# Kernel tuning notes

Hardware: AMD Instinct MI355X
Metric: run time of the kernel (lower is better)

The kernel has to match this reference:

```python
import jax, jax.numpy as jnp
import numpy as np

SENT_LEN, SENT_BATCH, WORD_LEN = 256, 64, 16
EMB, HID = 128, 256
CEMB, CHID = 64, 128
VOCAB, CVOCAB, TAGS = 50000, 128, 50


def setup_inputs() -> dict:
    key = jax.random.key(0)
    ks = jax.random.split(key, 14)
    s = 0.1  # param init scale, avoids gate saturation
    n = lambda k, shape: (jax.random.normal(k, shape, dtype=jnp.float32) * s)
    return {
        "sentences": jax.random.randint(ks[0], (SENT_LEN, SENT_BATCH), 0, VOCAB),
        "words": jax.random.randint(ks[1], (SENT_BATCH, WORD_LEN, SENT_LEN), 0, CVOCAB),
        "char_embedding_dim": CEMB,
        "char_hidden_dim": CHID,
        "word_emb": n(ks[2], (VOCAB, EMB)),
        "char_emb": n(ks[3], (CVOCAB, CEMB)),
        "Wih_c": n(ks[4], (4 * CHID, CEMB)),
        "Whh_c": n(ks[5], (4 * CHID, CHID)),
        "bih_c": n(ks[6], (4 * CHID,)),
        "bhh_c": n(ks[7], (4 * CHID,)),
        "Wih_w": n(ks[8], (4 * HID, EMB + CHID)),
        "Whh_w": n(ks[9], (4 * HID, HID)),
        "bih_w": n(ks[10], (4 * HID,)),
        "bhh_w": n(ks[11], (4 * HID,)),
        "W_tag": n(ks[12], (TAGS, HID)),
        "b_tag": n(ks[13], (TAGS,)),
    }


def _lstm_cell(h, c, x, Wih, Whh, b):
    # torch gate order: input, forget, cell(g), output
    gates = x @ Wih.T + h @ Whh.T + b
    i, f, g, o = jnp.split(gates, 4, axis=-1)
    c_new = jax.nn.sigmoid(f) * c + jax.nn.sigmoid(i) * jnp.tanh(g)
    h_new = jax.nn.sigmoid(o) * jnp.tanh(c_new)
    return h_new, c_new


def reference(sentences, words, char_embedding_dim, char_hidden_dim,
              word_emb, char_emb, Wih_c, Whh_c, bih_c, bhh_c,
              Wih_w, Whh_w, bih_w, bhh_w, W_tag, b_tag):
    sent_len, sent_batch = sentences.shape
    dt = word_emb.dtype

    embeds = word_emb[sentences]            # [T, B, EMB]
    ce = char_emb[words]                    # [B, WL, T, CEMB]

    # char LSTM: per sentence, seq=WL, batch=T; hidden carried ACROSS sentences
    b_c = bih_c + bhh_c

    def char_sentence(carry, sent_ce):      # sent_ce: [WL, T, CEMB]
        def step(hc, x):
            h, c = _lstm_cell(hc[0], hc[1], x, Wih_c, Whh_c, b_c)
            return (h, c), None
        carry, _ = jax.lax.scan(step, carry, sent_ce)
        return carry, carry[0]               # final h: [T, CHID]

    init_c = (jnp.zeros((sent_len, CHID), dt), jnp.zeros((sent_len, CHID), dt))
    _, char_finals = jax.lax.scan(char_sentence, init_c, ce)  # [B, T, CHID]
    char_finals = jnp.transpose(char_finals, (1, 0, 2))        # [T, B, CHID]

    x = jnp.concatenate([embeds, char_finals], axis=-1)        # [T, B, EMB+CHID]

    # word LSTM over time=T, batch=B
    b_w = bih_w + bhh_w

    def word_step(hc, xt):
        h, c = _lstm_cell(hc[0], hc[1], xt, Wih_w, Whh_w, b_w)
        return (h, c), h

    init_w = (jnp.zeros((sent_batch, HID), dt), jnp.zeros((sent_batch, HID), dt))
    _, lstm_out = jax.lax.scan(word_step, init_w, x)           # [T, B, HID]

    tag_space = lstm_out @ W_tag.T + b_tag                     # [T, B, TAGS]
    return jax.nn.log_softmax(tag_space, axis=-1)
```

## Files before the change

### kernel.cpp

```cpp
#include <hip/hip_runtime.h>
#include <hip/hip_bf16.h>
#include <cstdint>

#define SENT_LEN   256
#define SENT_BATCH 64
#define WORD_LEN   16
#define EMB        128
#define HID        256
#define CEMB       64
#define CHID       128
#define TAGS       50
#define K_IN       (EMB + CHID)
#define LOG2E      1.44269504f
#define N2LOG2E    -2.88539008f

typedef __attribute__((ext_vector_type(8))) short short8;
typedef __attribute__((ext_vector_type(4))) float f32x4;
typedef __attribute__((ext_vector_type(4))) int   i32x4;
typedef __attribute__((ext_vector_type(2))) long  lng2;

__device__ __forceinline__ float rcpf(float x) { return __builtin_amdgcn_rcpf(x); }
__device__ __forceinline__ float sig2(float xl) {
    return rcpf(1.f + __builtin_amdgcn_exp2f(-xl));
}
__device__ __forceinline__ float tanh2(float xl) {
    float e = __builtin_amdgcn_exp2f(-(xl + xl));
    return 2.f * rcpf(1.f + e) - 1.f;
}
__device__ __forceinline__ float lstm_act(float gi, float gf, float gg, float go, float& cst) {
    float c = sig2(gf) * cst + sig2(gi) * tanh2(gg);
    cst = c;
    float tc = 2.f * rcpf(1.f + __builtin_amdgcn_exp2f(N2LOG2E * c)) - 1.f;
    return sig2(go) * tc;
}
__device__ __forceinline__ float bf_lo(unsigned u) { return __uint_as_float(u << 16); }
__device__ __forceinline__ float bf_hi(unsigned u) { return __uint_as_float(u & 0xffff0000u); }
__device__ __forceinline__ unsigned short f2bfu(float f) {
    unsigned u = __float_as_uint(f);
    u += 0x7fff + ((u >> 16) & 1);
    return (unsigned short)(u >> 16);
}
__device__ __forceinline__ void block_sync_lds() {
    asm volatile("s_waitcnt lgkmcnt(0)\ns_barrier" ::: "memory");
}
__device__ __forceinline__ i32x4 mfma_i8_k64(lng2 a, lng2 b, i32x4 c) {
    i32x4 av = __builtin_bit_cast(i32x4, a);
    i32x4 bv = __builtin_bit_cast(i32x4, b);
    return __builtin_amdgcn_mfma_i32_16x16x64_i8(av, bv, c, 0, 0, 0);
}
template<int Q> __device__ __forceinline__ float qbcast(float x) {
    return __int_as_float(__builtin_amdgcn_mov_dpp(
        __float_as_int(x), Q * 0x55, 0xF, 0xF, false));
}

__global__ void prep_char(const float* __restrict__ Wih_c, const float* __restrict__ char_emb,
                          const float* __restrict__ bih_c, const float* __restrict__ bhh_c,
                          float* __restrict__ pre8) {
    int ch = blockIdx.x;
    int g  = threadIdx.x;
    float acc = bih_c[g] + bhh_c[g];
    const float4* w4 = reinterpret_cast<const float4*>(Wih_c + (size_t)g * CEMB);
    const float4* e4 = reinterpret_cast<const float4*>(char_emb + (size_t)ch * CEMB);
#pragma unroll
    for (int k = 0; k < CEMB / 4; k++) {
        float4 wv = w4[k], ev = e4[k];
        acc += wv.x * ev.x; acc += wv.y * ev.y;
        acc += wv.z * ev.z; acc += wv.w * ev.w;
    }
    int gt = g >> 7, j = g & 127;
    float s_e = (gt == 2) ? -2.f : -1.f;
    pre8[((ch * 128) + j) * 4 + gt] = acc * LOG2E * s_e;
}

__global__ void prep_wq(const float* __restrict__ Whh_w, const float* __restrict__ Wih_w,
                        signed char* __restrict__ wq, float* __restrict__ sw,
                        unsigned short* __restrict__ wihb) {
    int g = blockIdx.x;
    int lane = threadIdx.x;
    float4 v = reinterpret_cast<const float4*>(Whh_w + (size_t)g * HID)[lane];
    float m = fmaxf(fmaxf(fabsf(v.x), fabsf(v.y)), fmaxf(fabsf(v.z), fabsf(v.w)));
#pragma unroll
    for (int off = 32; off; off >>= 1) m = fmaxf(m, __shfl_xor(m, off, 64));
    m = fmaxf(m, 1e-20f);
    float inv = 127.f / m;
    int q0 = __float2int_rn(v.x * inv), q1 = __float2int_rn(v.y * inv);
    int q2 = __float2int_rn(v.z * inv), q3 = __float2int_rn(v.w * inv);
    int packed = (q0 & 255) | ((q1 & 255) << 8) | ((q2 & 255) << 16) | ((q3 & 255) << 24);
    reinterpret_cast<int*>(wq)[g * 64 + lane] = packed;
    if (lane == 0) sw[g] = m / 127.f;
    float4 wv = reinterpret_cast<const float4*>(Wih_w + (size_t)g * K_IN)[lane];
    uint2 p;
    p.x = (unsigned)f2bfu(wv.x) | ((unsigned)f2bfu(wv.y) << 16);
    p.y = (unsigned)f2bfu(wv.z) | ((unsigned)f2bfu(wv.w) << 16);
    int n2 = g >> 8, j = g & 255, jt = j >> 4, l15 = j & 15;
    int k0 = lane * 4;
    int kt = k0 >> 5, lqf = (k0 >> 3) & 3;
    size_t fidx = ((size_t)(jt * 4 + n2) * 8 + kt) * 64 + (lqf * 16 + l15);
    char* dst = (char*)wihb + fidx * 16 + (size_t)(k0 & 4) * 2;
    *reinterpret_cast<uint2*>(dst) = p;
}

__global__ __launch_bounds__(512, 1) void char_lstm(
        const int* __restrict__ words, const float* __restrict__ Whh_c,
        const float* __restrict__ pre8, const int* __restrict__ sentences,
        const float* __restrict__ word_emb, const unsigned short* __restrict__ wihb,
        const float* __restrict__ bih_w, const float* __restrict__ bhh_w,
        uint2* __restrict__ xw8) {
    int t    = blockIdx.x;
    int tid  = threadIdx.x;
    int lane = tid & 63, w = tid >> 6;
    int nt   = lane & 3;
    int j    = w * 16 + (lane >> 2);
    int g    = nt * 128 + j;

    __shared__ __align__(16) signed char hv[2][128];
    __shared__ __align__(16) unsigned short xls[64][264];

    const float4* wr = reinterpret_cast<const float4*>(Whh_c + (size_t)g * CHID);
    float mx = 1e-20f;
#pragma unroll
    for (int q = 0; q < 32; q++) {
        float4 f = wr[q];
        mx = fmaxf(mx, fmaxf(fmaxf(fabsf(f.x), fabsf(f.y)), fmaxf(fabsf(f.z), fabsf(f.w))));
    }
    float inv = 127.f / mx;
    int wqr[32];
#pragma unroll
    for (int q = 0; q < 32; q++) {
        float4 f = wr[q];
        wqr[q] = (__float2int_rn(f.x * inv) & 255)
               | ((__float2int_rn(f.y * inv) & 255) << 8)
               | ((__float2int_rn(f.z * inv) & 255) << 16)
               | ((__float2int_rn(f.w * inv) & 255) << 24);
    }
    float s_e   = (nt == 2) ? -2.f : -1.f;
    float swl_s = s_e * mx * (LOG2E / (127.f * 127.f));
    float m_a   = (nt == 2) ?  2.f :  1.f;
    float b_a   = (nt == 2) ? -1.f :  0.f;

    {
        int b  = tid >> 3;
        int c8 = tid & 7;
        int sid = sentences[t * 64 + b];
        const float4* ep = reinterpret_cast<const float4*>(
            word_emb + (size_t)sid * EMB + c8 * 16);
        float4 e0 = ep[0], e1 = ep[1], e2 = ep[2], e3 = ep[3];
        short8 v0, v1;
        v0[0] = (short)f2bfu(e0.x); v0[1] = (short)f2bfu(e0.y);
        v0[2] = (short)f2bfu(e0.z); v0[3] = (short)f2bfu(e0.w);
        v0[4] = (short)f2bfu(e1.x); v0[5] = (short)f2bfu(e1.y);
        v0[6] = (short)f2bfu(e1.z); v0[7] = (short)f2bfu(e1.w);
        v1[0] = (short)f2bfu(e2.x); v1[1] = (short)f2bfu(e2.y);
        v1[2] = (short)f2bfu(e2.z); v1[3] = (short)f2bfu(e2.w);
        v1[4] = (short)f2bfu(e3.x); v1[5] = (short)f2bfu(e3.y);
        v1[6] = (short)f2bfu(e3.z); v1[7] = (short)f2bfu(e3.w);
        *reinterpret_cast<short8*>(&xls[b][c8 * 16])     = v0;
        *reinterpret_cast<short8*>(&xls[b][c8 * 16 + 8]) = v1;
    }

    if (tid < 64) { reinterpret_cast<int*>(hv)[tid] = 0; }

    float cst = 0.f;
    int cid0 = words[t];
    int cid1 = words[SENT_LEN + t];
    float pl0 = pre8[(size_t)cid0 * 512 + tid];
    float pl1 = pre8[(size_t)cid1 * 512 + tid];
    int ci2 = words[2 * SENT_LEN + t];
    int ci3 = words[3 * SENT_LEN + t];
    __syncthreads();

    for (int u = 0; u < 512; u++) {
        float pf0 = pre8[(size_t)ci2 * 512 + tid];
        float pf1 = pre8[(size_t)ci3 * 512 + tid];
        ci2 = words[(((u << 1) + 4) & 1023) * SENT_LEN + t];
        ci3 = words[(((u << 1) + 5) & 1023) * SENT_LEN + t];

        {
            const i32x4* hp = reinterpret_cast<const i32x4*>(hv[0]);
            int a0 = 0, a1 = 0, a2 = 0, a3 = 0;
#pragma unroll
            for (int q = 0; q < 8; q++) {
                i32x4 hq = hp[q];
                a0 = __builtin_amdgcn_sdot4(hq.x, wqr[q * 4 + 0], a0, false);
                a1 = __builtin_amdgcn_sdot4(hq.y, wqr[q * 4 + 1], a1, false);
                a2 = __builtin_amdgcn_sdot4(hq.z, wqr[q * 4 + 2], a2, false);
                a3 = __builtin_amdgcn_sdot4(hq.w, wqr[q * 4 + 3], a3, false);
            }
            int s = (a0 + a1) + (a2 + a3);
            float e  = __builtin_amdgcn_exp2f(fmaf((float)s, swl_s, pl0));
            float av = m_a * rcpf(1.f + e) + b_a;
            float qi = qbcast<0>(av);
            float qf = qbcast<1>(av);
            float qg = qbcast<2>(av);
            float qo = qbcast<3>(av);
            float c  = fmaf(qf, cst, qi * qg);
            cst = c;
            float tc = 2.f * rcpf(1.f + __builtin_amdgcn_exp2f(N2LOG2E * c)) - 1.f;
            float h  = qo * tc;
            if (nt == 0)
                hv[1][j] = (signed char)__float2int_rn(h * 127.f);
            block_sync_lds();
        }
        {
            const i32x4* hp = reinterpret_cast<const i32x4*>(hv[1]);
            int a0 = 0, a1 = 0, a2 = 0, a3 = 0;
#pragma unroll
            for (int q = 0; q < 8; q++) {
                i32x4 hq = hp[q];
                a0 = __builtin_amdgcn_sdot4(hq.x, wqr[q * 4 + 0], a0, false);
                a1 = __builtin_amdgcn_sdot4(hq.y, wqr[q * 4 + 1], a1, false);
                a2 = __builtin_amdgcn_sdot4(hq.z, wqr[q * 4 + 2], a2, false);
                a3 = __builtin_amdgcn_sdot4(hq.w, wqr[q * 4 + 3], a3, false);
            }
            int s = (a0 + a1) + (a2 + a3);
            float e  = __builtin_amdgcn_exp2f(fmaf((float)s, swl_s, pl1));
            float av = m_a * rcpf(1.f + e) + b_a;
            float qi = qbcast<0>(av);
            float qf = qbcast<1>(av);
            float qg = qbcast<2>(av);
            float qo = qbcast<3>(av);
            float c  = fmaf(qf, cst, qi * qg);
            cst = c;
            float tc = 2.f * rcpf(1.f + __builtin_amdgcn_exp2f(N2LOG2E * c)) - 1.f;
            float h  = qo * tc;
            if (nt == 0) {
                hv[0][j] = (signed char)__float2int_rn(h * 127.f);
                if ((u & 7) == 7)
                    xls[u >> 3][128 + j] = f2bfu(h);
            }
            block_sync_lds();
        }
        pl0 = pf0; pl1 = pf1;
    }

    {
        int l15 = lane & 15, lq = lane >> 4;
        int mt  = w & 3;
        short8 af[8];
#pragma unroll
        for (int kt = 0; kt < 8; kt++)
            af[kt] = *reinterpret_cast<const short8*>(&xls[mt * 16 + l15][kt * 32 + lq * 8]);
        const short8* bF = reinterpret_cast<const short8*>(wihb);
#pragma unroll 1
        for (int jt = (w >> 2); jt < 16; jt += 2) {
            int j0 = jt * 16;
            const short8* bJ = bF + (size_t)jt * 4 * 8 * 64 + lane;
            f32x4 acc[4] = {{0.f,0.f,0.f,0.f},{0.f,0.f,0.f,0.f},
                            {0.f,0.f,0.f,0.f},{0.f,0.f,0.f,0.f}};
#pragma unroll
            for (int kt = 0; kt < 8; kt++) {
#pragma unroll
                for (int n2 = 0; n2 < 4; n2++) {
                    short8 bf = bJ[(n2 * 8 + kt) * 64];
                    acc[n2] = __builtin_amdgcn_mfma_f32_16x16x32_bf16(
                        af[kt], bf, acc[n2], 0, 0, 0);
                }
            }
            float bb[4];
#pragma unroll
            for (int n2 = 0; n2 < 4; n2++)
                bb[n2] = bih_w[n2 * 256 + j0 + l15] + bhh_w[n2 * 256 + j0 + l15];
#pragma unroll
            for (int r = 0; r < 4; r++) {
                int br = mt * 16 + lq * 4 + r;
                uint2 o;
                o.x = (unsigned)f2bfu((acc[0][r] + bb[0]) * LOG2E)
                    | ((unsigned)f2bfu((acc[1][r] + bb[1]) * LOG2E) << 16);
                o.y = (unsigned)f2bfu((acc[2][r] + bb[2]) * LOG2E)
                    | ((unsigned)f2bfu((acc[3][r] + bb[3]) * LOG2E) << 16);
                xw8[((size_t)br * SENT_LEN + t) * 256 + j0 + l15] = o;
            }
        }
    }
}

__global__ __launch_bounds__(1024, 1) void word_lstm(
        const uint2* __restrict__ xw8, const signed char* __restrict__ wq,
        const float* __restrict__ sw, float* __restrict__ h_out) {
    int b    = blockIdx.x;
    int tid  = threadIdx.x;
    int lane = tid & 63, w = tid >> 6;
    int l15  = lane & 15, lq = lane >> 4;
    int j    = w * 16 + l15;

    __shared__ __align__(16) signed char hv[2][256];

    lng2 bfr[4][4];
    float swl[4];
#pragma unroll
    for (int nt = 0; nt < 4; nt++) {
        int g = nt * 256 + j;
        swl[nt] = sw[g] * (LOG2E / 127.f);
#pragma unroll
        for (int kt = 0; kt < 4; kt++)
            bfr[nt][kt] = reinterpret_cast<const lng2*>(wq + (size_t)g * HID + kt * 64 + lq * 16)[0];
    }
    if (tid < 128) { reinterpret_cast<int*>(hv)[tid] = 0; }

    const uint2* xwb = xw8 + (size_t)b * SENT_LEN * 256;
    float cst = 0.f;
    uint2 xq0 = xwb[0 * 256 + j];
    uint2 xq1 = xwb[1 * 256 + j];
    uint2 xq2 = xwb[2 * 256 + j];
    uint2 xq3 = xwb[3 * 256 + j];
    __syncthreads();

    for (int u = 0; u < 128; u++) {
        uint2 xn0 = xwb[((((u << 1) + 4) & 255)) * 256 + j];
        uint2 xn1 = xwb[((((u << 1) + 5) & 255)) * 256 + j];

        {
            const lng2* hp = reinterpret_cast<const lng2*>(hv[0]);
            i32x4 acc[4] = {};
#pragma unroll
            for (int kt = 0; kt < 4; kt++) {
                lng2 a = hp[kt * 4 + lq];
#pragma unroll
                for (int nt = 0; nt < 4; nt++)
                    acc[nt] = mfma_i8_k64(a, bfr[nt][kt], acc[nt]);
            }
            float gi = (float)acc[0][0] * swl[0] + bf_lo(xq0.x);
            float gf = (float)acc[1][0] * swl[1] + bf_hi(xq0.x);
            float gg = (float)acc[2][0] * swl[2] + bf_lo(xq0.y);
            float go = (float)acc[3][0] * swl[3] + bf_hi(xq0.y);
            float h = lstm_act(gi, gf, gg, go, cst);
            if (lq == 0) {
                h_out[((size_t)(u << 1) * SENT_BATCH + b) * HID + j] = h;
                hv[1][j] = (signed char)__float2int_rn(h * 127.f);
            }
            block_sync_lds();
        }
        {
            const lng2* hp = reinterpret_cast<const lng2*>(hv[1]);
            i32x4 acc[4] = {};
#pragma unroll
            for (int kt = 0; kt < 4; kt++) {
                lng2 a = hp[kt * 4 + lq];
#pragma unroll
                for (int nt = 0; nt < 4; nt++)
                    acc[nt] = mfma_i8_k64(a, bfr[nt][kt], acc[nt]);
            }
            float gi = (float)acc[0][0] * swl[0] + bf_lo(xq1.x);
            float gf = (float)acc[1][0] * swl[1] + bf_hi(xq1.x);
            float gg = (float)acc[2][0] * swl[2] + bf_lo(xq1.y);
            float go = (float)acc[3][0] * swl[3] + bf_hi(xq1.y);
            float h = lstm_act(gi, gf, gg, go, cst);
            if (lq == 0) {
                h_out[((size_t)((u << 1) + 1) * SENT_BATCH + b) * HID + j] = h;
                hv[0][j] = (signed char)__float2int_rn(h * 127.f);
            }
            block_sync_lds();
        }
        xq0 = xq2; xq1 = xq3; xq2 = xn0; xq3 = xn1;
    }
}

__global__ __launch_bounds__(256) void tag_logsoftmax(
        const float* __restrict__ h_out, const float* __restrict__ W_tag,
        const float* __restrict__ b_tag, float* __restrict__ out) {
    __shared__ float wt_s[TAGS * 257];
    __shared__ float hr_s[8 * HID];
    int tid = threadIdx.x;
    int row0 = blockIdx.x * 8;
#pragma unroll 2
    for (int i = 0; i < TAGS; i++) wt_s[i * 257 + tid] = W_tag[i * HID + tid];
#pragma unroll
    for (int w = 0; w < 8; w++) hr_s[w * HID + tid] = h_out[(size_t)(row0 + w) * HID + tid];
    __syncthreads();

    int w4 = tid >> 6, l = tid & 63;
#pragma unroll
    for (int rep = 0; rep < 2; rep++) {
        int w = rep * 4 + w4;
        float acc = 0.f;
        if (l < TAGS) {
            acc = b_tag[l];
            const float* hr = hr_s + w * HID;
            const float* wr = wt_s + l * 257;
#pragma unroll 4
            for (int k = 0; k < HID; k++) acc += hr[k] * wr[k];
        }
        float m = (l < TAGS) ? acc : -1e30f;
#pragma unroll
        for (int off = 32; off; off >>= 1) m = fmaxf(m, __shfl_xor(m, off, 64));
        float e = (l < TAGS) ? __builtin_amdgcn_exp2f((acc - m) * LOG2E) : 0.f;
        float ssum = e;
#pragma unroll
        for (int off = 32; off; off >>= 1) ssum += __shfl_xor(ssum, off, 64);
        float lse = m + __logf(ssum);
        if (l < TAGS) out[(size_t)(row0 + w) * TAGS + l] = acc - lse;
    }
}

extern "C" void kernel_launch(void* const* d_in, const int* in_sizes, int n_in,
                              void* d_out, int out_size, void* d_ws, size_t ws_size,
                              hipStream_t stream) {
    (void)in_sizes; (void)n_in; (void)out_size; (void)ws_size;
    const int*   sentences = (const int*)d_in[0];
    const int*   words     = (const int*)d_in[1];
    const float* word_emb  = (const float*)d_in[4];
    const float* char_emb  = (const float*)d_in[5];
    const float* Wih_c     = (const float*)d_in[6];
    const float* Whh_c     = (const float*)d_in[7];
    const float* bih_c     = (const float*)d_in[8];
    const float* bhh_c     = (const float*)d_in[9];
    const float* Wih_w     = (const float*)d_in[10];
    const float* Whh_w     = (const float*)d_in[11];
    const float* bih_w     = (const float*)d_in[12];
    const float* bhh_w     = (const float*)d_in[13];
    const float* W_tag     = (const float*)d_in[14];
    const float* b_tag     = (const float*)d_in[15];
    float* out = (float*)d_out;

    char* ws = (char*)d_ws;
    size_t off = 0;
    float* pre8 = (float*)(ws + off);                 off += 128 * 512 * sizeof(float);
    signed char* wq = (signed char*)(ws + off);       off += 1024 * 256;
    float* sw = (float*)(ws + off);                   off += 1024 * sizeof(float);
    unsigned short* wihb = (unsigned short*)(ws + off); off += (size_t)1024 * K_IN * 2;
    off = (off + 255) & ~(size_t)255;
    uint2* xw8 = (uint2*)(ws + off);                  off += (size_t)SENT_LEN * SENT_BATCH * 256 * sizeof(uint2);
    float* h_out = (float*)(ws + off);                off += (size_t)SENT_LEN * SENT_BATCH * HID * sizeof(float);

    hipLaunchKernelGGL(prep_char, dim3(128), dim3(512), 0, stream,
                       Wih_c, char_emb, bih_c, bhh_c, pre8);
    hipLaunchKernelGGL(prep_wq, dim3(1024), dim3(64), 0, stream, Whh_w, Wih_w, wq, sw, wihb);
    hipLaunchKernelGGL(char_lstm, dim3(256), dim3(512), 0, stream,
                       words, Whh_c, pre8, sentences, word_emb, wihb, bih_w, bhh_w, xw8);
    hipLaunchKernelGGL(word_lstm, dim3(SENT_BATCH), dim3(1024), 0, stream,
                       xw8, wq, sw, h_out);
    hipLaunchKernelGGL(tag_logsoftmax, dim3((SENT_LEN * SENT_BATCH) / 8), dim3(256), 0, stream,
                       h_out, W_tag, b_tag, out);
}
```

Before: 808.8 us.

## Halve word LSTM block to 512 threads with two hidden units per thread; merge prep kernels

The word LSTM block shrinks from 1024 to 512 threads, and each thread now computes two hidden units (j and j+128). That doubles the MFMAs and register-held weights per wave but halves the number of waves meeting at each per-timestep barrier. The two weight-prep kernels are also merged into one launch, with the Whh quantisation now packing 8 gate rows per block instead of one. The intent is to cut barrier cost on the serial recurrence and save one launch, at the price of more register pressure and a longer serial chain of work per wave.

```diff
diff --git a/kernel.cpp b/kernel.cpp
--- a/kernel.cpp
+++ b/kernel.cpp
@@ -53,51 +53,53 @@
         __float_as_int(x), Q * 0x55, 0xF, 0xF, false));
 }
 
-__global__ void prep_char(const float* __restrict__ Wih_c, const float* __restrict__ char_emb,
-                          const float* __restrict__ bih_c, const float* __restrict__ bhh_c,
-                          float* __restrict__ pre8) {
-    int ch = blockIdx.x;
-    int g  = threadIdx.x;
-    float acc = bih_c[g] + bhh_c[g];
-    const float4* w4 = reinterpret_cast<const float4*>(Wih_c + (size_t)g * CEMB);
-    const float4* e4 = reinterpret_cast<const float4*>(char_emb + (size_t)ch * CEMB);
-#pragma unroll
-    for (int k = 0; k < CEMB / 4; k++) {
-        float4 wv = w4[k], ev = e4[k];
-        acc += wv.x * ev.x; acc += wv.y * ev.y;
-        acc += wv.z * ev.z; acc += wv.w * ev.w;
-    }
-    int gt = g >> 7, j = g & 127;
-    float s_e = (gt == 2) ? -2.f : -1.f;
-    pre8[((ch * 128) + j) * 4 + gt] = acc * LOG2E * s_e;
-}
-
-__global__ void prep_wq(const float* __restrict__ Whh_w, const float* __restrict__ Wih_w,
-                        signed char* __restrict__ wq, float* __restrict__ sw,
-                        unsigned short* __restrict__ wihb) {
-    int g = blockIdx.x;
-    int lane = threadIdx.x;
-    float4 v = reinterpret_cast<const float4*>(Whh_w + (size_t)g * HID)[lane];
-    float m = fmaxf(fmaxf(fabsf(v.x), fabsf(v.y)), fmaxf(fabsf(v.z), fabsf(v.w)));
-#pragma unroll
-    for (int off = 32; off; off >>= 1) m = fmaxf(m, __shfl_xor(m, off, 64));
-    m = fmaxf(m, 1e-20f);
-    float inv = 127.f / m;
-    int q0 = __float2int_rn(v.x * inv), q1 = __float2int_rn(v.y * inv);
-    int q2 = __float2int_rn(v.z * inv), q3 = __float2int_rn(v.w * inv);
-    int packed = (q0 & 255) | ((q1 & 255) << 8) | ((q2 & 255) << 16) | ((q3 & 255) << 24);
-    reinterpret_cast<int*>(wq)[g * 64 + lane] = packed;
-    if (lane == 0) sw[g] = m / 127.f;
-    float4 wv = reinterpret_cast<const float4*>(Wih_w + (size_t)g * K_IN)[lane];
-    uint2 p;
-    p.x = (unsigned)f2bfu(wv.x) | ((unsigned)f2bfu(wv.y) << 16);
-    p.y = (unsigned)f2bfu(wv.z) | ((unsigned)f2bfu(wv.w) << 16);
-    int n2 = g >> 8, j = g & 255, jt = j >> 4, l15 = j & 15;
-    int k0 = lane * 4;
-    int kt = k0 >> 5, lqf = (k0 >> 3) & 3;
-    size_t fidx = ((size_t)(jt * 4 + n2) * 8 + kt) * 64 + (lqf * 16 + l15);
-    char* dst = (char*)wihb + fidx * 16 + (size_t)(k0 & 4) * 2;
-    *reinterpret_cast<uint2*>(dst) = p;
+__global__ __launch_bounds__(512) void prep_all(
+        const float* __restrict__ Wih_c, const float* __restrict__ char_emb,
+        const float* __restrict__ bih_c, const float* __restrict__ bhh_c,
+        const float* __restrict__ Whh_w, const float* __restrict__ Wih_w,
+        float* __restrict__ pre8, signed char* __restrict__ wq,
+        float* __restrict__ sw, unsigned short* __restrict__ wihb) {
+    int bid = blockIdx.x;
+    int tid = threadIdx.x;
+    if (bid < 128) {
+        int ch = bid, g = tid;
+        float acc = bih_c[g] + bhh_c[g];
+        const float4* w4 = reinterpret_cast<const float4*>(Wih_c + (size_t)g * CEMB);
+        const float4* e4 = reinterpret_cast<const float4*>(char_emb + (size_t)ch * CEMB);
+#pragma unroll
+        for (int k = 0; k < CEMB / 4; k++) {
+            float4 wv = w4[k], ev = e4[k];
+            acc += wv.x * ev.x; acc += wv.y * ev.y;
+            acc += wv.z * ev.z; acc += wv.w * ev.w;
+        }
+        int gt = g >> 7, j = g & 127;
+        float s_e = (gt == 2) ? -2.f : -1.f;
+        pre8[((ch * 128) + j) * 4 + gt] = acc * LOG2E * s_e;
+    } else {
+        int g = (bid - 128) * 8 + (tid >> 6);
+        int lane = tid & 63;
+        float4 v = reinterpret_cast<const float4*>(Whh_w + (size_t)g * HID)[lane];
+        float m = fmaxf(fmaxf(fabsf(v.x), fabsf(v.y)), fmaxf(fabsf(v.z), fabsf(v.w)));
+#pragma unroll
+        for (int off = 32; off; off >>= 1) m = fmaxf(m, __shfl_xor(m, off, 64));
+        m = fmaxf(m, 1e-20f);
+        float inv = 127.f / m;
+        int q0 = __float2int_rn(v.x * inv), q1 = __float2int_rn(v.y * inv);
+        int q2 = __float2int_rn(v.z * inv), q3 = __float2int_rn(v.w * inv);
+        int packed = (q0 & 255) | ((q1 & 255) << 8) | ((q2 & 255) << 16) | ((q3 & 255) << 24);
+        reinterpret_cast<int*>(wq)[g * 64 + lane] = packed;
+        if (lane == 0) sw[g] = m / 127.f;
+        float4 wv = reinterpret_cast<const float4*>(Wih_w + (size_t)g * K_IN)[lane];
+        uint2 p;
+        p.x = (unsigned)f2bfu(wv.x) | ((unsigned)f2bfu(wv.y) << 16);
+        p.y = (unsigned)f2bfu(wv.z) | ((unsigned)f2bfu(wv.w) << 16);
+        int n2 = g >> 8, j = g & 255, jt = j >> 4, l15 = j & 15;
+        int k0 = lane * 4;
+        int kt = k0 >> 5, lqf = (k0 >> 3) & 3;
+        size_t fidx = ((size_t)(jt * 4 + n2) * 8 + kt) * 64 + (lqf * 16 + l15);
+        char* dst = (char*)wihb + fidx * 16 + (size_t)(k0 & 4) * 2;
+        *reinterpret_cast<uint2*>(dst) = p;
+    }
 }
 
 __global__ __launch_bounds__(512, 1) void char_lstm(
@@ -274,84 +276,109 @@
     }
 }
 
-__global__ __launch_bounds__(1024, 1) void word_lstm(
+__global__ __launch_bounds__(512, 1) void word_lstm(
         const uint2* __restrict__ xw8, const signed char* __restrict__ wq,
         const float* __restrict__ sw, float* __restrict__ h_out) {
     int b    = blockIdx.x;
     int tid  = threadIdx.x;
     int lane = tid & 63, w = tid >> 6;
     int l15  = lane & 15, lq = lane >> 4;
-    int j    = w * 16 + l15;
+    int j0   = w * 16 + l15;
+    int j1   = j0 + 128;
 
     __shared__ __align__(16) signed char hv[2][256];
 
-    lng2 bfr[4][4];
-    float swl[4];
+    lng2 bfr0[4][4], bfr1[4][4];
+    float swl0[4], swl1[4];
 #pragma unroll
     for (int nt = 0; nt < 4; nt++) {
-        int g = nt * 256 + j;
-        swl[nt] = sw[g] * (LOG2E / 127.f);
-#pragma unroll
-        for (int kt = 0; kt < 4; kt++)
-            bfr[nt][kt] = reinterpret_cast<const lng2*>(wq + (size_t)g * HID + kt * 64 + lq * 16)[0];
+        int g0 = nt * 256 + j0, g1 = nt * 256 + j1;
+        swl0[nt] = sw[g0] * (LOG2E / 127.f);
+        swl1[nt] = sw[g1] * (LOG2E / 127.f);
+#pragma unroll
+        for (int kt = 0; kt < 4; kt++) {
+            bfr0[nt][kt] = reinterpret_cast<const lng2*>(wq + (size_t)g0 * HID + kt * 64 + lq * 16)[0];
+            bfr1[nt][kt] = reinterpret_cast<const lng2*>(wq + (size_t)g1 * HID + kt * 64 + lq * 16)[0];
+        }
     }
     if (tid < 128) { reinterpret_cast<int*>(hv)[tid] = 0; }
 
     const uint2* xwb = xw8 + (size_t)b * SENT_LEN * 256;
-    float cst = 0.f;
-    uint2 xq0 = xwb[0 * 256 + j];
-    uint2 xq1 = xwb[1 * 256 + j];
-    uint2 xq2 = xwb[2 * 256 + j];
-    uint2 xq3 = xwb[3 * 256 + j];
+    float cst0 = 0.f, cst1 = 0.f;
+    uint2 xa0 = xwb[0 * 256 + j0], xb0 = xwb[0 * 256 + j1];
+    uint2 xa1 = xwb[1 * 256 + j0], xb1 = xwb[1 * 256 + j1];
+    uint2 xa2 = xwb[2 * 256 + j0], xb2 = xwb[2 * 256 + j1];
+    uint2 xa3 = xwb[3 * 256 + j0], xb3 = xwb[3 * 256 + j1];
     __syncthreads();
 
     for (int u = 0; u < 128; u++) {
-        uint2 xn0 = xwb[((((u << 1) + 4) & 255)) * 256 + j];
-        uint2 xn1 = xwb[((((u << 1) + 5) & 255)) * 256 + j];
+        uint2 xn0 = xwb[((((u << 1) + 4) & 255)) * 256 + j0];
+        uint2 xm0 = xwb[((((u << 1) + 4) & 255)) * 256 + j1];
+        uint2 xn1 = xwb[((((u << 1) + 5) & 255)) * 256 + j0];
+        uint2 xm1 = xwb[((((u << 1) + 5) & 255)) * 256 + j1];
 
         {
             const lng2* hp = reinterpret_cast<const lng2*>(hv[0]);
-            i32x4 acc[4] = {};
+            i32x4 ac0[4] = {}, ac1[4] = {};
 #pragma unroll
             for (int kt = 0; kt < 4; kt++) {
                 lng2 a = hp[kt * 4 + lq];
 #pragma unroll
-                for (int nt = 0; nt < 4; nt++)
-                    acc[nt] = mfma_i8_k64(a, bfr[nt][kt], acc[nt]);
-            }
-            float gi = (float)acc[0][0] * swl[0] + bf_lo(xq0.x);
-            float gf = (float)acc[1][0] * swl[1] + bf_hi(xq0.x);
-            float gg = (float)acc[2][0] * swl[2] + bf_lo(xq0.y);
-            float go = (float)acc[3][0] * swl[3] + bf_hi(xq0.y);
-            float h = lstm_act(gi, gf, gg, go, cst);
+                for (int nt = 0; nt < 4; nt++) {
+                    ac0[nt] = mfma_i8_k64(a, bfr0[nt][kt], ac0[nt]);
+                    ac1[nt] = mfma_i8_k64(a, bfr1[nt][kt], ac1[nt]);
+                }
+            }
+            float gi0 = (float)ac0[0][0] * swl0[0] + bf_lo(xa0.x);
+            float gf0 = (float)ac0[1][0] * swl0[1] + bf_hi(xa0.x);
+            float gg0 = (float)ac0[2][0] * swl0[2] + bf_lo(xa0.y);
+            float go0 = (float)ac0[3][0] * swl0[3] + bf_hi(xa0.y);
+            float h0 = lstm_act(gi0, gf0, gg0, go0, cst0);
+            float gi1 = (float)ac1[0][0] * swl1[0] + bf_lo(xb0.x);
+            float gf1 = (float)ac1[1][0] * swl1[1] + bf_hi(xb0.x);
+            float gg1 = (float)ac1[2][0] * swl1[2] + bf_lo(xb0.y);
+            float go1 = (float)ac1[3][0] * swl1[3] + bf_hi(xb0.y);
+            float h1 = lstm_act(gi1, gf1, gg1, go1, cst1);
             if (lq == 0) {
-                h_out[((size_t)(u << 1) * SENT_BATCH + b) * HID + j] = h;
-                hv[1][j] = (signed char)__float2int_rn(h * 127.f);
+                h_out[((size_t)(u << 1) * SENT_BATCH + b) * HID + j0] = h0;
+                h_out[((size_t)(u << 1) * SENT_BATCH + b) * HID + j1] = h1;
+                hv[1][j0] = (signed char)__float2int_rn(h0 * 127.f);
+                hv[1][j1] = (signed char)__float2int_rn(h1 * 127.f);
             }
             block_sync_lds();
         }
         {
             const lng2* hp = reinterpret_cast<const lng2*>(hv[1]);
-            i32x4 acc[4] = {};
+            i32x4 ac0[4] = {}, ac1[4] = {};
 #pragma unroll
             for (int kt = 0; kt < 4; kt++) {
                 lng2 a = hp[kt * 4 + lq];
 #pragma unroll
-                for (int nt = 0; nt < 4; nt++)
-                    acc[nt] = mfma_i8_k64(a, bfr[nt][kt], acc[nt]);
-            }
-            float gi = (float)acc[0][0] * swl[0] + bf_lo(xq1.x);
-            float gf = (float)acc[1][0] * swl[1] + bf_hi(xq1.x);
-            float gg = (float)acc[2][0] * swl[2] + bf_lo(xq1.y);
-            float go = (float)acc[3][0] * swl[3] + bf_hi(xq1.y);
-            float h = lstm_act(gi, gf, gg, go, cst);
+                for (int nt = 0; nt < 4; nt++) {
+                    ac0[nt] = mfma_i8_k64(a, bfr0[nt][kt], ac0[nt]);
+                    ac1[nt] = mfma_i8_k64(a, bfr1[nt][kt], ac1[nt]);
+                }
+            }
+            float gi0 = (float)ac0[0][0] * swl0[0] + bf_lo(xa1.x);
+            float gf0 = (float)ac0[1][0] * swl0[1] + bf_hi(xa1.x);
+            float gg0 = (float)ac0[2][0] * swl0[2] + bf_lo(xa1.y);
+            float go0 = (float)ac0[3][0] * swl0[3] + bf_hi(xa1.y);
+            float h0 = lstm_act(gi0, gf0, gg0, go0, cst0);
+            float gi1 = (float)ac1[0][0] * swl1[0] + bf_lo(xb1.x);
+            float gf1 = (float)ac1[1][0] * swl1[1] + bf_hi(xb1.x);
+            float gg1 = (float)ac1[2][0] * swl1[2] + bf_lo(xb1.y);
+            float go1 = (float)ac1[3][0] * swl1[3] + bf_hi(xb1.y);
+            float h1 = lstm_act(gi1, gf1, gg1, go1, cst1);
             if (lq == 0) {
-                h_out[((size_t)((u << 1) + 1) * SENT_BATCH + b) * HID + j] = h;
-                hv[0][j] = (signed char)__float2int_rn(h * 127.f);
+                h_out[((size_t)((u << 1) + 1) * SENT_BATCH + b) * HID + j0] = h0;
+                h_out[((size_t)((u << 1) + 1) * SENT_BATCH + b) * HID + j1] = h1;
+                hv[0][j0] = (signed char)__float2int_rn(h0 * 127.f);
+                hv[0][j1] = (signed char)__float2int_rn(h1 * 127.f);
             }
             block_sync_lds();
         }
-        xq0 = xq2; xq1 = xq3; xq2 = xn0; xq3 = xn1;
+        xa0 = xa2; xb0 = xb2; xa1 = xa3; xb1 = xb3;
+        xa2 = xn0; xb2 = xm0; xa3 = xn1; xb3 = xm1;
     }
 }
 
@@ -422,12 +449,12 @@
     uint2* xw8 = (uint2*)(ws + off);                  off += (size_t)SENT_LEN * SENT_BATCH * 256 * sizeof(uint2);
     float* h_out = (float*)(ws + off);                off += (size_t)SENT_LEN * SENT_BATCH * HID * sizeof(float);
 
-    hipLaunchKernelGGL(prep_char, dim3(128), dim3(512), 0, stream,
-                       Wih_c, char_emb, bih_c, bhh_c, pre8);
-    hipLaunchKernelGGL(prep_wq, dim3(1024), dim3(64), 0, stream, Whh_w, Wih_w, wq, sw, wihb);
+    hipLaunchKernelGGL(prep_all, dim3(256), dim3(512), 0, stream,
+                       Wih_c, char_emb, bih_c, bhh_c, Whh_w, Wih_w,
+                       pre8, wq, sw, wihb);
     hipLaunchKernelGGL(char_lstm, dim3(256), dim3(512), 0, stream,
                        words, Whh_c, pre8, sentences, word_emb, wihb, bih_w, bhh_w, xw8);
-    hipLaunchKernelGGL(word_lstm, dim3(SENT_BATCH), dim3(1024), 0, stream,
+    hipLaunchKernelGGL(word_lstm, dim3(SENT_BATCH), dim3(512), 0, stream,
                        xw8, wq, sw, h_out);
     hipLaunchKernelGGL(tag_logsoftmax, dim3((SENT_LEN * SENT_BATCH) / 8), dim3(256), 0, stream,
                        h_out, W_tag, b_tag, out);
```

Result: slower. 846.4 us (+4.7%).
